# Performance work log

Measured on AMD Instinct MI355X. Metric: run time of the kernel, lower is better.

The kernel has to match this reference:

```python
import jax, jax.numpy as jnp
import numpy as np

N_FREQ = 256
N_CH = 256
VOCAB = 8192
B, T = 4, 2048


def gauss_proj(x, w, n_freq):
    # FFT over vocab dim, take first n_freq harmonics (skip DC), split real/imag
    X = jnp.fft.rfft(x, axis=-1)[..., 1:n_freq + 1]          # [B,T,n_freq] complex
    X_ri = jnp.concatenate([X.real, X.imag], axis=-1)         # [B,T,2*n_freq]
    return X_ri @ w.T                                         # [B,T,n_channels]


def gauss_synth(h, w, n_freq, V):
    Y_ri = h @ w                                              # [B,T,2*n_freq]
    Y = Y_ri[..., :n_freq] + 1j * Y_ri[..., n_freq:]          # [B,T,n_freq] complex
    full = jnp.zeros(h.shape[:-1] + (V // 2 + 1,), dtype=Y.dtype)
    full = full.at[..., 1:n_freq + 1].set(Y)                  # band-limited spectrum
    return jnp.fft.irfft(full, n=V, axis=-1)                  # [B,T,V]


def setup_inputs() -> dict:
    key = jax.random.key(0)
    ks = jax.random.split(key, 5)
    x = jax.random.normal(ks[0], (B, T, VOCAB), dtype=jnp.float32)
    q_w = jax.random.normal(ks[1], (N_CH, 2 * N_FREQ), dtype=jnp.float32) * 0.02
    k_w = jax.random.normal(ks[2], (N_CH, 2 * N_FREQ), dtype=jnp.float32) * 0.02
    v_w = jax.random.normal(ks[3], (N_CH, 2 * N_FREQ), dtype=jnp.float32) * 0.02
    o_w = jax.random.normal(ks[4], (N_CH, 2 * N_FREQ), dtype=jnp.float32) * 0.02
    decay_logit = jnp.float32(3.0)
    out_scale = jnp.float32(0.1)
    return {"x": x, "q_w": q_w, "k_w": k_w, "v_w": v_w, "o_w": o_w,
            "decay_logit": decay_logit, "out_scale": out_scale}


def reference(x, q_w, k_w, v_w, o_w, decay_logit, out_scale):
    q = gauss_proj(x, q_w, N_FREQ)                            # [B,T,C]
    k = gauss_proj(x, k_w, N_FREQ)
    v = gauss_proj(x, v_w, N_FREQ)
    scores = jnp.einsum('btc,bsc->bts', q, k)                 # [B,T,T]
    decay = jax.nn.sigmoid(decay_logit)
    t = x.shape[1]
    pos = jnp.arange(t)
    # faithful to torch: diff[t,s] = pos[s] - pos[t]
    diff = pos[None, :] - pos[:, None]
    weights = (decay ** jnp.clip(diff.astype(jnp.float32) - 1.0, 0.0)) * (diff > 0)
    scores = scores * weights[None, :, :]
    retrieved = jnp.einsum('bts,bsc->btc', scores, v)         # [B,T,C]
    return gauss_synth(retrieved, o_w, N_FREQ, VOCAB) * out_scale
```

## Files before the change

### kernel.cpp

```cpp
#include <hip/hip_runtime.h>
#include <hip/hip_bf16.h>
#include <cstdint>


typedef unsigned short u16;
typedef short short8 __attribute__((ext_vector_type(8)));
typedef float f32x4 __attribute__((ext_vector_type(4)));
typedef float f4 __attribute__((ext_vector_type(4)));

__device__ __forceinline__ u16 f2bf(float f) {
  union { float f; unsigned u; } v; v.f = f;
  unsigned u = v.u;
  u += 0x7fffu + ((u >> 16) & 1u);
  return (u16)(u >> 16);
}

__device__ __forceinline__ uint2 pack_bf4(f4 v) {
  union { u16 h[4]; uint2 q; } pk;
  pk.h[0] = f2bf(v[0]); pk.h[1] = f2bf(v[1]);
  pk.h[2] = f2bf(v[2]); pk.h[3] = f2bf(v[3]);
  return pk.q;
}

__device__ __forceinline__ void gload_lds16(const void* g, void* l) {
  __builtin_amdgcn_global_load_lds(
      (const __attribute__((address_space(1))) void*)g,
      (__attribute__((address_space(3))) void*)l, 16, 0, 0);
}

__global__ __launch_bounds__(256, 2)
void gemm_g1(const float* __restrict__ A, const u16* __restrict__ B,
             float* __restrict__ P)
{
  constexpr int NN = 512, KK = 8192, KC = 4096;
  constexpr int NT = KC / 64;

  __shared__ u16 As[2][128 * 64] __attribute__((aligned(16)));
  __shared__ u16 Bs[2][128 * 64] __attribute__((aligned(16)));

  const int tid  = threadIdx.x;
  const int wave = tid >> 6, lane = tid & 63;
  const int quad = lane >> 4, l15 = lane & 15;
  const int wm = wave >> 1, wn = wave & 1;
  const int swz8 = (l15 & 7) << 3;

  const int lid = blockIdx.x;
  const int nat = (lid & 7) * 64 + (lid >> 3);
  const int y = nat >> 3, rem = nat & 7;
  const int x = rem & 3, z = rem >> 2;
  const int m0 = y * 128, n0 = x * 128, k00 = z * KC;

  const int brow = tid >> 3;
  const int bswz = ((tid & 7) * 8) ^ (((tid >> 3) & 7) << 3);
  const u16* Bp = B + (size_t)(n0 + brow) * KK + k00 + bswz;
  const int bloff = tid * 16;

  const int arow16 = tid >> 4;
  const int acolf  = (tid & 15) * 4;
  const float* Ap = A + (size_t)(m0 + arow16) * KK + k00 + acolf;
  const int awz = ((tid & 15) * 4) ^ (((tid >> 4) & 7) << 3);

  f4 rv0[8], rv1[8];

#define ISSUE_A(RV, T)                                               \
  _Pragma("unroll")                                                  \
  for (int g = 0; g < 8; ++g)                                        \
    RV[g] = *(const f4*)(Ap + (size_t)g * 16 * KK + (size_t)(T) * 64);
#define ISSUE_B(T, SLOT)                                             \
  _Pragma("unroll")                                                  \
  for (int h = 0; h < 4; ++h)                                        \
    gload_lds16(Bp + (size_t)h * 32 * KK + (size_t)(T) * 64,         \
                (char*)Bs[SLOT] + h * 4096 + bloff);
#define CONVERT_A(RV, SLOT)                                          \
  _Pragma("unroll")                                                  \
  for (int g = 0; g < 8; ++g)                                        \
    *(uint2*)&As[SLOT][(g * 16 + arow16) * 64 + awz] = pack_bf4(RV[g]);
#define G1_COMPUTE(CUR)                                                          \
  _Pragma("unroll")                                                              \
  for (int ks = 0; ks < 2; ++ks) {                                               \
    short8 a[4], b[4];                                                           \
    _Pragma("unroll")                                                            \
    for (int i = 0; i < 4; ++i)                                                  \
      a[i] = *(const short8*)&As[CUR][(wm * 64 + i * 16 + l15) * 64 +            \
                                      ((ks * 32 + quad * 8) ^ swz8)];            \
    _Pragma("unroll")                                                            \
    for (int j = 0; j < 4; ++j)                                                  \
      b[j] = *(const short8*)&Bs[CUR][(wn * 64 + j * 16 + l15) * 64 +            \
                                      ((ks * 32 + quad * 8) ^ swz8)];            \
    _Pragma("unroll")                                                            \
    for (int i = 0; i < 4; ++i)                                                  \
      _Pragma("unroll")                                                          \
      for (int j = 0; j < 4; ++j)                                                \
        acc[i][j] = __builtin_amdgcn_mfma_f32_16x16x32_bf16(a[i], b[j], acc[i][j], 0, 0, 0); \
  }
#define SB() __builtin_amdgcn_sched_barrier(0)
#define FENCE_BAR()                                                  \
  asm volatile("s_waitcnt vmcnt(8)" ::: "memory");                   \
  asm volatile("s_waitcnt lgkmcnt(0)" ::: "memory");                 \
  __builtin_amdgcn_s_barrier();                                      \
  asm volatile("" ::: "memory");

  ISSUE_A(rv0, 0);
  ISSUE_B(0, 0);
  SB();
  ISSUE_A(rv1, 1);
  SB();
  CONVERT_A(rv0, 0);
  FENCE_BAR();

  f32x4 acc[4][4] = {};

#define BODY(T, RV_ISS, RV_CONV)                                     \
  {                                                                  \
    const int t2 = ((T) + 2 < NT) ? (T) + 2 : NT - 1;                \
    ISSUE_B((T) + 1 < NT ? (T) + 1 : NT - 1, ((T) + 1) & 1);         \
    SB();                                                            \
    ISSUE_A(RV_ISS, t2);                                             \
    SB();                                                            \
    G1_COMPUTE((T) & 1);                                             \
    CONVERT_A(RV_CONV, ((T) + 1) & 1);                               \
    FENCE_BAR();                                                     \
  }

  for (int t = 0; t < NT; t += 2) {
    BODY(t, rv0, rv1);
    BODY(t + 1, rv1, rv0);
  }
#undef BODY
#undef FENCE_BAR
#undef SB
#undef G1_COMPUTE
#undef CONVERT_A
#undef ISSUE_B
#undef ISSUE_A

  float* Pz = P + (size_t)z * (8192L * 512);
  #pragma unroll
  for (int i = 0; i < 4; ++i) {
    #pragma unroll
    for (int j = 0; j < 4; ++j) {
      const int rb = m0 + wm * 64 + i * 16 + quad * 4;
      const int cc = n0 + wn * 64 + j * 16 + l15;
      #pragma unroll
      for (int r = 0; r < 4; ++r)
        Pz[(size_t)(rb + r) * NN + cc] = acc[i][j][r];
    }
  }
}

__global__ void reduce_cast(const float* __restrict__ P, u16* __restrict__ O,
                            int half_f4) {
  const int i = blockIdx.x * 256 + threadIdx.x;
  const f4 a = ((const f4*)P)[i];
  const f4 b = ((const f4*)P)[i + half_f4];
  union { u16 h[4]; uint2 q; } pk;
  #pragma unroll
  for (int r = 0; r < 4; ++r) pk.h[r] = f2bf(a[r] + b[r]);
  ((uint2*)O)[i] = pk.q;
}

__device__ __forceinline__ void kloop_p(
    const u16* __restrict__ Ab, const u16* __restrict__ Bb, int K,
    int m0, int n0, int kbeg, int kend, int tid,
    u16* As, u16* Bs, f32x4 (&acc)[4][4])
{
  const int wave = tid >> 6, lane = tid & 63;
  const int quad = lane >> 4, l15 = lane & 15;
  const int wm = wave >> 1, wn = wave & 1;
  const int swz8 = (l15 & 7) << 3;

  const int brow = tid >> 3;
  const int rswz = ((tid & 7) * 8) ^ ((brow & 7) << 3);
  const u16* Apg = Ab + (size_t)(m0 + brow) * K + rswz;
  const u16* Bpg = Bb + (size_t)(n0 + brow) * K + rswz;
  const int dof = tid * 16;

#define STG_P(K0, SLOT)                                                     \
  _Pragma("unroll")                                                         \
  for (int h = 0; h < 4; ++h) {                                             \
    gload_lds16(Apg + (size_t)h * 32 * K + (K0),                            \
                (char*)As + (SLOT) * 16384 + h * 4096 + dof);               \
    gload_lds16(Bpg + (size_t)h * 32 * K + (K0),                            \
                (char*)Bs + (SLOT) * 16384 + h * 4096 + dof);               \
  }

  STG_P(kbeg, 0);
  asm volatile("s_waitcnt vmcnt(0)" ::: "memory");
  __builtin_amdgcn_s_barrier();
  asm volatile("" ::: "memory");

  int buf = 0;
  for (int k0 = kbeg; k0 < kend; k0 += 64) {
    if (k0 + 64 < kend) STG_P(k0 + 64, buf ^ 1);
    #pragma unroll
    for (int ks = 0; ks < 2; ++ks) {
      short8 a[4], b[4];
      #pragma unroll
      for (int i = 0; i < 4; ++i)
        a[i] = *(const short8*)&As[buf * 8192 + (wm * 64 + i * 16 + l15) * 64 +
                                   ((ks * 32 + quad * 8) ^ swz8)];
      #pragma unroll
      for (int j = 0; j < 4; ++j)
        b[j] = *(const short8*)&Bs[buf * 8192 + (wn * 64 + j * 16 + l15) * 64 +
                                   ((ks * 32 + quad * 8) ^ swz8)];
      #pragma unroll
      for (int i = 0; i < 4; ++i)
        #pragma unroll
        for (int j = 0; j < 4; ++j)
          acc[i][j] = __builtin_amdgcn_mfma_f32_16x16x32_bf16(a[i], b[j], acc[i][j], 0, 0, 0);
    }
    asm volatile("s_waitcnt vmcnt(0)" ::: "memory");
    __builtin_amdgcn_s_barrier();
    asm volatile("" ::: "memory");
    buf ^= 1;
  }
#undef STG_P
}

__global__ __launch_bounds__(256, 2)
void gemm_qkvw(const u16* __restrict__ Xri, const u16* __restrict__ Fm,
               const u16* __restrict__ qwb, const u16* __restrict__ kwb,
               const u16* __restrict__ vwb, const u16* __restrict__ owb,
               u16* __restrict__ Qb, u16* __restrict__ Kb,
               u16* __restrict__ Vt, u16* __restrict__ Wot)
{
  constexpr int N = 256, K = 512;
  __shared__ u16 As[2 * 128 * 64] __attribute__((aligned(16)));
  __shared__ u16 Bs[2 * 128 * 64] __attribute__((aligned(16)));

  const int tid  = threadIdx.x;
  const int wave = tid >> 6, lane = tid & 63;
  const int quad = lane >> 4, l15 = lane & 15;
  const int wm = wave >> 1, wn = wave & 1;
  const int m0 = blockIdx.y * 128, n0 = blockIdx.x * 128;
  const int z  = blockIdx.z;

  const u16* Ab = (z == 3) ? Fm : Xri;
  const u16* Bb = (z == 0) ? qwb : (z == 1) ? kwb : (z == 2) ? vwb : owb;
  const float alpha = (z == 3) ? (2.f / 8192.f) : 1.f;

  f32x4 acc[4][4] = {};
  kloop_p(Ab, Bb, K, m0, n0, 0, K, tid, As, Bs, acc);

  #pragma unroll
  for (int i = 0; i < 4; ++i) {
    #pragma unroll
    for (int j = 0; j < 4; ++j) {
      f32x4 v = acc[i][j];
      const int rb = m0 + wm * 64 + i * 16 + quad * 4;
      const int cc = n0 + wn * 64 + j * 16 + l15;
      if (z == 2) {
        const int bb = rb >> 11, ml = rb & 2047;
        union { u16 h[4]; uint2 q; } pk;
        #pragma unroll
        for (int r = 0; r < 4; ++r) pk.h[r] = f2bf(v[r]);
        *(uint2*)&Vt[((size_t)(bb << 8) + cc) * 2048 + ml] = pk.q;
      } else {
        u16* C = (z == 0) ? Qb : (z == 1) ? Kb : Wot;
        #pragma unroll
        for (int r = 0; r < 4; ++r)
          C[(size_t)(rb + r) * N + cc] = f2bf(v[r] * alpha);
      }
    }
  }
}

__global__ __launch_bounds__(256, 2)
void gemm_g4(const u16* __restrict__ Qb, const u16* __restrict__ Kb,
             u16* __restrict__ S, const float* __restrict__ dl)
{
  if (blockIdx.x < blockIdx.y) return;
  constexpr int N = 2048, K = 256;
  __shared__ u16 As[2 * 128 * 64] __attribute__((aligned(16)));
  __shared__ u16 Bs[2 * 128 * 64] __attribute__((aligned(16)));

  const int tid  = threadIdx.x;
  const int wave = tid >> 6, lane = tid & 63;
  const int quad = lane >> 4, l15 = lane & 15;
  const int wm = wave >> 1, wn = wave & 1;
  const int m0 = blockIdx.y * 128, n0 = blockIdx.x * 128;
  const int z  = blockIdx.z;

  const u16* Ab = Qb + (size_t)z * 2048 * 256;
  const u16* Bb = Kb + (size_t)z * 2048 * 256;

  f32x4 acc[4][4] = {};
  kloop_p(Ab, Bb, K, m0, n0, 0, K, tid, As, Bs, acc);

  const float logit = *dl;
  const float dec = 1.f / (1.f + expf(-logit));
  const float dec_l2 = log2f(dec);
  u16* C = S + (size_t)z * 2048 * 2048;

  #pragma unroll
  for (int i = 0; i < 4; ++i) {
    #pragma unroll
    for (int j = 0; j < 4; ++j) {
      f32x4 v = acc[i][j];
      const int rb = m0 + wm * 64 + i * 16 + quad * 4;
      const int cc = n0 + wn * 64 + j * 16 + l15;
      #pragma unroll
      for (int r = 0; r < 4; ++r) {
        const int d = cc - (rb + r);
        float w = (d > 0) ? exp2f(dec_l2 * (float)(d - 1)) : 0.f;
        C[(size_t)(rb + r) * N + cc] = f2bf(v[r] * w);
      }
    }
  }
}

__global__ __launch_bounds__(256, 2)
void gemm_g5(const u16* __restrict__ S, const u16* __restrict__ Vt,
             float* __restrict__ P5)
{
  constexpr int N = 256, K = 2048;
  __shared__ u16 As[2 * 128 * 64] __attribute__((aligned(16)));
  __shared__ u16 Bs[2 * 128 * 64] __attribute__((aligned(16)));

  const int tid  = threadIdx.x;
  const int wave = tid >> 6, lane = tid & 63;
  const int quad = lane >> 4, l15 = lane & 15;
  const int wm = wave >> 1, wn = wave & 1;
  const int m0 = blockIdx.y * 128, n0 = blockIdx.x * 128;
  const int batch = blockIdx.z & 3, half = blockIdx.z >> 2;

  const u16* Ab = S  + (size_t)batch * 2048 * 2048;
  const u16* Bb = Vt + (size_t)batch * 256 * 2048;

  int kbeg = half * 1024;
  if (m0 > kbeg) kbeg = m0;
  const int kend = half * 1024 + 1024;

  f32x4 acc[4][4] = {};
  if (kbeg < kend)
    kloop_p(Ab, Bb, K, m0, n0, kbeg, kend, tid, As, Bs, acc);

  float* Pz = P5 + (size_t)half * (8192L * 256) + (size_t)batch * 2048 * 256;
  #pragma unroll
  for (int i = 0; i < 4; ++i) {
    #pragma unroll
    for (int j = 0; j < 4; ++j) {
      const int rb = m0 + wm * 64 + i * 16 + quad * 4;
      const int cc = n0 + wn * 64 + j * 16 + l15;
      #pragma unroll
      for (int r = 0; r < 4; ++r)
        Pz[(size_t)(rb + r) * N + cc] = acc[i][j][r];
    }
  }
}

__global__ __launch_bounds__(256, 2)
void gemm_g6(const u16* __restrict__ R, const u16* __restrict__ Wot,
             float* __restrict__ out, const float* __restrict__ os)
{
  constexpr int N = 8192, K = 256;
  __shared__ u16 As[2 * 128 * 64] __attribute__((aligned(16)));
  __shared__ u16 Bs[2 * 128 * 64] __attribute__((aligned(16)));

  const int tid  = threadIdx.x;
  const int wave = tid >> 6, lane = tid & 63;
  const int quad = lane >> 4, l15 = lane & 15;
  const int wm = wave >> 1, wn = wave & 1;
  const int m0 = blockIdx.y * 128, n0 = blockIdx.x * 128;

  f32x4 acc[4][4] = {};
  kloop_p(R, Wot, K, m0, n0, 0, K, tid, As, Bs, acc);

  const float oscale = *os;
  #pragma unroll
  for (int i = 0; i < 4; ++i) {
    #pragma unroll
    for (int j = 0; j < 4; ++j) {
      const int rb = m0 + wm * 64 + i * 16 + quad * 4;
      const int cc = n0 + wn * 64 + j * 16 + l15;
      #pragma unroll
      for (int r = 0; r < 4; ++r)
        out[(size_t)(rb + r) * N + cc] = acc[i][j][r] * oscale;
    }
  }
}

__global__ void genF_row(u16* Fm) {
  int idx = blockIdx.x * 256 + threadIdx.x;
  int n = idx >> 9, j = idx & 511;
  int k = (j & 255) + 1;
  int ph = (n * k) & 8191;
  float ang = (float)ph * 7.66990393942820795e-4f;
  float s, c; sincosf(ang, &s, &c);
  Fm[idx] = f2bf(j < 256 ? c : -s);
}
__global__ void genF_col(u16* Ft) {
  int idx = blockIdx.x * 256 + threadIdx.x;
  int j = idx >> 13, n = idx & 8191;
  int k = (j & 255) + 1;
  int ph = (n * k) & 8191;
  float ang = (float)ph * 7.66990393942820795e-4f;
  float s, c; sincosf(ang, &s, &c);
  Ft[idx] = f2bf(j < 256 ? c : -s);
}

__global__ void cast_w4(const float* a, const float* b, const float* c, const float* d,
                        u16* oa, u16* ob, u16* oc, u16* od) {
  int i = blockIdx.x * 256 + threadIdx.x;
  oa[i] = f2bf(a[i]); ob[i] = f2bf(b[i]); oc[i] = f2bf(c[i]); od[i] = f2bf(d[i]);
}

extern "C" void kernel_launch(void* const* d_in, const int* in_sizes, int n_in,
                              void* d_out, int out_size, void* d_ws, size_t ws_size,
                              hipStream_t stream)
{
  const float* x  = (const float*)d_in[0];
  const float* qw = (const float*)d_in[1];
  const float* kw = (const float*)d_in[2];
  const float* vw = (const float*)d_in[3];
  const float* ow = (const float*)d_in[4];
  const float* dl = (const float*)d_in[5];
  const float* os = (const float*)d_in[6];
  float* out = (float*)d_out;

  char* W = (char*)d_ws;
  const size_t MB = 1024 * 1024;
  u16* Fm  = (u16*)(W);
  u16* Ft  = (u16*)(W + 8 * MB);
  u16* Xri = (u16*)(W + 16 * MB);
  u16* Qb  = (u16*)(W + 24 * MB);
  u16* Kb  = (u16*)(W + 28 * MB);
  u16* Vt  = (u16*)(W + 32 * MB);
  u16* Wot = (u16*)(W + 36 * MB);
  u16* S   = (u16*)(W + 40 * MB);
  float* P = (float*)(W + 40 * MB);
  float* P5 = (float*)(W);
  u16* R   = (u16*)(W + 72 * MB);
  u16* qwb = (u16*)(W + 76 * MB);
  u16* kwb = qwb + 131072;
  u16* vwb = kwb + 131072;
  u16* owb = vwb + 131072;

  genF_row<<<8192 * 512 / 256, 256, 0, stream>>>(Fm);
  genF_col<<<8192 * 512 / 256, 256, 0, stream>>>(Ft);
  cast_w4<<<131072 / 256, 256, 0, stream>>>(qw, kw, vw, ow, qwb, kwb, vwb, owb);

  gemm_g1<<<512, 256, 0, stream>>>(x, Ft, P);
  reduce_cast<<<4096, 256, 0, stream>>>(P, Xri, 8192 * 512 / 4);

  gemm_qkvw<<<dim3(2, 64, 4), 256, 0, stream>>>(Xri, Fm, qwb, kwb, vwb, owb,
                                                Qb, Kb, Vt, Wot);

  gemm_g4<<<dim3(16, 16, 4), 256, 0, stream>>>(Qb, Kb, S, dl);

  gemm_g5<<<dim3(2, 16, 8), 256, 0, stream>>>(S, Vt, P5);
  reduce_cast<<<2048, 256, 0, stream>>>(P5, R, 8192 * 256 / 4);

  gemm_g6<<<dim3(64, 64, 1), 256, 0, stream>>>(R, Wot, out, os);
}
```

Measured before the change: 622.6 us.

## Load A fragments directly into registers in gemm_g1 and merge prep kernels

The first GEMM no longer stages the fp32 x tile through LDS as bf16. Each wave now loads its own A rows straight into registers and converts them into MFMA fragments. The K step drops from 64 to 32, shared memory holds only the B double buffer, and the launch bound rises to 3 blocks per CU. The DFT matrix generation and weight casting kernels are merged into one launch to cut launch overhead. In exchange, A rows are reloaded redundantly by the two waves sharing wm, there are twice as many barriers, and there is less prefetch depth for A.

```diff
diff --git a/kernel.cpp b/kernel.cpp
--- a/kernel.cpp
+++ b/kernel.cpp
@@ -15,34 +15,25 @@
   return (u16)(u >> 16);
 }
 
-__device__ __forceinline__ uint2 pack_bf4(f4 v) {
-  union { u16 h[4]; uint2 q; } pk;
-  pk.h[0] = f2bf(v[0]); pk.h[1] = f2bf(v[1]);
-  pk.h[2] = f2bf(v[2]); pk.h[3] = f2bf(v[3]);
-  return pk.q;
-}
-
 __device__ __forceinline__ void gload_lds16(const void* g, void* l) {
   __builtin_amdgcn_global_load_lds(
       (const __attribute__((address_space(1))) void*)g,
       (__attribute__((address_space(3))) void*)l, 16, 0, 0);
 }
 
-__global__ __launch_bounds__(256, 2)
+__global__ __launch_bounds__(256, 3)
 void gemm_g1(const float* __restrict__ A, const u16* __restrict__ B,
              float* __restrict__ P)
 {
   constexpr int NN = 512, KK = 8192, KC = 4096;
-  constexpr int NT = KC / 64;
-
-  __shared__ u16 As[2][128 * 64] __attribute__((aligned(16)));
-  __shared__ u16 Bs[2][128 * 64] __attribute__((aligned(16)));
+  constexpr int NT = KC / 32;
+
+  __shared__ u16 Bs[2][128 * 32] __attribute__((aligned(16)));
 
   const int tid  = threadIdx.x;
   const int wave = tid >> 6, lane = tid & 63;
   const int quad = lane >> 4, l15 = lane & 15;
   const int wm = wave >> 1, wn = wave & 1;
-  const int swz8 = (l15 & 7) << 3;
 
   const int lid = blockIdx.x;
   const int nat = (lid & 7) * 64 + (lid >> 3);
@@ -50,89 +41,82 @@
   const int x = rem & 3, z = rem >> 2;
   const int m0 = y * 128, n0 = x * 128, k00 = z * KC;
 
-  const int brow = tid >> 3;
-  const int bswz = ((tid & 7) * 8) ^ (((tid >> 3) & 7) << 3);
-  const u16* Bp = B + (size_t)(n0 + brow) * KK + k00 + bswz;
+  const int brow4 = tid >> 2;
+  const int bcol  = ((tid & 3) * 8) ^ ((brow4 & 3) * 8);
+  const u16* Bp = B + (size_t)(n0 + brow4) * KK + k00 + bcol;
   const int bloff = tid * 16;
 
-  const int arow16 = tid >> 4;
-  const int acolf  = (tid & 15) * 4;
-  const float* Ap = A + (size_t)(m0 + arow16) * KK + k00 + acolf;
-  const int awz = ((tid & 15) * 4) ^ (((tid >> 4) & 7) << 3);
-
-  f4 rv0[8], rv1[8];
-
-#define ISSUE_A(RV, T)                                               \
-  _Pragma("unroll")                                                  \
-  for (int g = 0; g < 8; ++g)                                        \
-    RV[g] = *(const f4*)(Ap + (size_t)g * 16 * KK + (size_t)(T) * 64);
+  const float* Ap = A + (size_t)(m0 + wm * 64 + l15) * KK + k00 + quad * 8;
+
+  const int swzB = (l15 & 3) * 8;
+
+  f4 rv[8];
+  short8 af[4];
+  f32x4 acc[4][4] = {};
+
 #define ISSUE_B(T, SLOT)                                             \
   _Pragma("unroll")                                                  \
-  for (int h = 0; h < 4; ++h)                                        \
-    gload_lds16(Bp + (size_t)h * 32 * KK + (size_t)(T) * 64,         \
+  for (int h = 0; h < 2; ++h)                                        \
+    gload_lds16(Bp + (size_t)h * 64 * KK + (size_t)(T) * 32,         \
                 (char*)Bs[SLOT] + h * 4096 + bloff);
-#define CONVERT_A(RV, SLOT)                                          \
+#define ISSUE_A(T)                                                   \
   _Pragma("unroll")                                                  \
-  for (int g = 0; g < 8; ++g)                                        \
-    *(uint2*)&As[SLOT][(g * 16 + arow16) * 64 + awz] = pack_bf4(RV[g]);
+  for (int i = 0; i < 4; ++i) {                                      \
+    rv[2 * i]     = *(const f4*)(Ap + (size_t)i * 16 * KK + (size_t)(T) * 32);     \
+    rv[2 * i + 1] = *(const f4*)(Ap + (size_t)i * 16 * KK + (size_t)(T) * 32 + 4); \
+  }
+#define CONVERT_A()                                                  \
+  _Pragma("unroll")                                                  \
+  for (int i = 0; i < 4; ++i) {                                      \
+    union { u16 h[8]; short8 s; } pk;                                \
+    _Pragma("unroll")                                                \
+    for (int e = 0; e < 4; ++e) {                                    \
+      pk.h[e]     = f2bf(rv[2 * i][e]);                              \
+      pk.h[4 + e] = f2bf(rv[2 * i + 1][e]);                          \
+    }                                                                \
+    af[i] = pk.s;                                                    \
+  }
 #define G1_COMPUTE(CUR)                                                          \
-  _Pragma("unroll")                                                              \
-  for (int ks = 0; ks < 2; ++ks) {                                               \
-    short8 a[4], b[4];                                                           \
-    _Pragma("unroll")                                                            \
-    for (int i = 0; i < 4; ++i)                                                  \
-      a[i] = *(const short8*)&As[CUR][(wm * 64 + i * 16 + l15) * 64 +            \
-                                      ((ks * 32 + quad * 8) ^ swz8)];            \
+  {                                                                              \
+    short8 b[4];                                                                 \
     _Pragma("unroll")                                                            \
     for (int j = 0; j < 4; ++j)                                                  \
-      b[j] = *(const short8*)&Bs[CUR][(wn * 64 + j * 16 + l15) * 64 +            \
-                                      ((ks * 32 + quad * 8) ^ swz8)];            \
+      b[j] = *(const short8*)&Bs[CUR][(wn * 64 + j * 16 + l15) * 32 +            \
+                                      ((quad * 8) ^ swzB)];                      \
     _Pragma("unroll")                                                            \
     for (int i = 0; i < 4; ++i)                                                  \
       _Pragma("unroll")                                                          \
       for (int j = 0; j < 4; ++j)                                                \
-        acc[i][j] = __builtin_amdgcn_mfma_f32_16x16x32_bf16(a[i], b[j], acc[i][j], 0, 0, 0); \
+        acc[i][j] = __builtin_amdgcn_mfma_f32_16x16x32_bf16(af[i], b[j], acc[i][j], 0, 0, 0); \
   }
 #define SB() __builtin_amdgcn_sched_barrier(0)
 #define FENCE_BAR()                                                  \
   asm volatile("s_waitcnt vmcnt(8)" ::: "memory");                   \
-  asm volatile("s_waitcnt lgkmcnt(0)" ::: "memory");                 \
   __builtin_amdgcn_s_barrier();                                      \
   asm volatile("" ::: "memory");
 
-  ISSUE_A(rv0, 0);
   ISSUE_B(0, 0);
   SB();
-  ISSUE_A(rv1, 1);
+  ISSUE_A(0);
   SB();
-  CONVERT_A(rv0, 0);
   FENCE_BAR();
 
-  f32x4 acc[4][4] = {};
-
-#define BODY(T, RV_ISS, RV_CONV)                                     \
-  {                                                                  \
-    const int t2 = ((T) + 2 < NT) ? (T) + 2 : NT - 1;                \
-    ISSUE_B((T) + 1 < NT ? (T) + 1 : NT - 1, ((T) + 1) & 1);         \
-    SB();                                                            \
-    ISSUE_A(RV_ISS, t2);                                             \
-    SB();                                                            \
-    G1_COMPUTE((T) & 1);                                             \
-    CONVERT_A(RV_CONV, ((T) + 1) & 1);                               \
-    FENCE_BAR();                                                     \
-  }
-
-  for (int t = 0; t < NT; t += 2) {
-    BODY(t, rv0, rv1);
-    BODY(t + 1, rv1, rv0);
-  }
-#undef BODY
+  for (int t = 0; t < NT; ++t) {
+    const int tn = (t + 1 < NT) ? t + 1 : NT - 1;
+    ISSUE_B(tn, (t + 1) & 1);
+    SB();
+    CONVERT_A();
+    ISSUE_A(tn);
+    SB();
+    G1_COMPUTE(t & 1);
+    FENCE_BAR();
+  }
 #undef FENCE_BAR
 #undef SB
 #undef G1_COMPUTE
 #undef CONVERT_A
+#undef ISSUE_A
 #undef ISSUE_B
-#undef ISSUE_A
 
   float* Pz = P + (size_t)z * (8192L * 512);
   #pragma unroll
@@ -380,29 +364,34 @@
   }
 }
 
-__global__ void genF_row(u16* Fm) {
-  int idx = blockIdx.x * 256 + threadIdx.x;
-  int n = idx >> 9, j = idx & 511;
-  int k = (j & 255) + 1;
-  int ph = (n * k) & 8191;
-  float ang = (float)ph * 7.66990393942820795e-4f;
-  float s, c; sincosf(ang, &s, &c);
-  Fm[idx] = f2bf(j < 256 ? c : -s);
-}
-__global__ void genF_col(u16* Ft) {
-  int idx = blockIdx.x * 256 + threadIdx.x;
-  int j = idx >> 13, n = idx & 8191;
-  int k = (j & 255) + 1;
-  int ph = (n * k) & 8191;
-  float ang = (float)ph * 7.66990393942820795e-4f;
-  float s, c; sincosf(ang, &s, &c);
-  Ft[idx] = f2bf(j < 256 ? c : -s);
-}
-
-__global__ void cast_w4(const float* a, const float* b, const float* c, const float* d,
-                        u16* oa, u16* ob, u16* oc, u16* od) {
-  int i = blockIdx.x * 256 + threadIdx.x;
-  oa[i] = f2bf(a[i]); ob[i] = f2bf(b[i]); oc[i] = f2bf(c[i]); od[i] = f2bf(d[i]);
+__global__ void prep(u16* __restrict__ Fm, u16* __restrict__ Ft,
+                     const float* __restrict__ qw, const float* __restrict__ kw,
+                     const float* __restrict__ vw, const float* __restrict__ ow,
+                     u16* __restrict__ qwb, u16* __restrict__ kwb,
+                     u16* __restrict__ vwb, u16* __restrict__ owb)
+{
+  const int b = blockIdx.x;
+  if (b < 16384) {
+    int idx = b * 256 + threadIdx.x;
+    int n = idx >> 9, j = idx & 511;
+    int k = (j & 255) + 1;
+    int ph = (n * k) & 8191;
+    float ang = (float)ph * 7.66990393942820795e-4f;
+    float s, c; sincosf(ang, &s, &c);
+    Fm[idx] = f2bf(j < 256 ? c : -s);
+  } else if (b < 32768) {
+    int idx = (b - 16384) * 256 + threadIdx.x;
+    int j = idx >> 13, n = idx & 8191;
+    int k = (j & 255) + 1;
+    int ph = (n * k) & 8191;
+    float ang = (float)ph * 7.66990393942820795e-4f;
+    float s, c; sincosf(ang, &s, &c);
+    Ft[idx] = f2bf(j < 256 ? c : -s);
+  } else {
+    int i = (b - 32768) * 256 + threadIdx.x;
+    qwb[i] = f2bf(qw[i]); kwb[i] = f2bf(kw[i]);
+    vwb[i] = f2bf(vw[i]); owb[i] = f2bf(ow[i]);
+  }
 }
 
 extern "C" void kernel_launch(void* const* d_in, const int* in_sizes, int n_in,
@@ -436,9 +425,7 @@
   u16* vwb = kwb + 131072;
   u16* owb = vwb + 131072;
 
-  genF_row<<<8192 * 512 / 256, 256, 0, stream>>>(Fm);
-  genF_col<<<8192 * 512 / 256, 256, 0, stream>>>(Ft);
-  cast_w4<<<131072 / 256, 256, 0, stream>>>(qw, kw, vw, ow, qwb, kwb, vwb, owb);
+  prep<<<33280, 256, 0, stream>>>(Fm, Ft, qw, kw, vw, ow, qwb, kwb, vwb, owb);
 
   gemm_g1<<<512, 256, 0, stream>>>(x, Ft, P);
   reduce_cast<<<4096, 256, 0, stream>>>(P, Xri, 8192 * 512 / 4);
```

New measurement: 761.3 us. 22.3% more time.
